# Performance work log

Measured on AMD Instinct MI355X. Metric: run time of the kernel, lower is better.

## Reference

```python
import jax, jax.numpy as jnp
import numpy as np

B, M, H, R = 4096, 4, 1024, 10
MID, D3 = 512, 3 * H  # gate MLP mid = max(32, H//2)
AUDIO = 1
OTHERS = (0, 2, 3)


def _ln(x, w, b):
    m = jnp.mean(x, axis=-1, keepdims=True)
    v = jnp.mean((x - m) ** 2, axis=-1, keepdims=True)
    return (x - m) * jax.lax.rsqrt(v + 1e-5) * w + b


def _gate(t, s, lw, lb, w1, b1, w2, b2):
    feat = jnp.concatenate([t, s, jnp.abs(t - s)], axis=-1)  # [..., 3H]
    h = jax.nn.gelu(_ln(feat, lw, lb) @ w1.T + b1, approximate=False)
    return jax.nn.sigmoid(h @ w2.T + b2)  # [..., 1]


def setup_inputs() -> dict:
    key = jax.random.key(0)
    ks = jax.random.split(key, 16)
    xn = lambda k, shp, fan: jax.random.normal(k, shp, jnp.float32) * (1.0 / np.sqrt(fan))
    inp = {
        'tokens': jax.random.normal(ks[0], (B, M, H), jnp.float32),
        'token_mask': jax.random.randint(ks[1], (B, M), 0, 2) > 0,
        # gate_other: LayerNorm(3H) -> Linear(3H,MID) -> GELU -> Linear(MID,1)
        'ln_go_w': jnp.ones((D3,), jnp.float32), 'ln_go_b': jnp.zeros((D3,), jnp.float32),
        'go_w1': xn(ks[2], (MID, D3), D3), 'go_b1': jnp.zeros((MID,), jnp.float32),
        'go_w2': xn(ks[3], (1, MID), MID), 'go_b2': jnp.zeros((1,), jnp.float32),
        # gate_audio
        'ln_ga_w': jnp.ones((D3,), jnp.float32), 'ln_ga_b': jnp.zeros((D3,), jnp.float32),
        'ga_w1': xn(ks[4], (MID, D3), D3), 'ga_b1': jnp.zeros((MID,), jnp.float32),
        'ga_w2': xn(ks[5], (1, MID), MID), 'ga_b2': jnp.zeros((1,), jnp.float32),
        'a2o_w': xn(ks[6], (H, H), H), 'o2a_w': xn(ks[7], (H, H), H),
        'ln_o_w': jnp.ones((H,), jnp.float32), 'ln_o_b': jnp.zeros((H,), jnp.float32),
        'ln_a_w': jnp.ones((H,), jnp.float32), 'ln_a_b': jnp.zeros((H,), jnp.float32),
        # LMF
        'factors': jax.random.normal(ks[8], (M, R, H + 1, H), jnp.float32) * np.sqrt(2.0 / (H + 1 + H)),
        'rank_w': jax.random.normal(ks[9], (R,), jnp.float32) * 0.02,
        'lmf_bias': jnp.zeros((H,), jnp.float32),
        'out_ln1_w': jnp.ones((H,), jnp.float32), 'out_ln1_b': jnp.zeros((H,), jnp.float32),
        'out_w': xn(ks[10], (H, H), H), 'out_b': jnp.zeros((H,), jnp.float32),
        'out_ln2_w': jnp.ones((H,), jnp.float32), 'out_ln2_b': jnp.zeros((H,), jnp.float32),
    }
    return inp


def reference(tokens, token_mask, ln_go_w, ln_go_b, go_w1, go_b1, go_w2, go_b2,
              ln_ga_w, ln_ga_b, ga_w1, ga_b1, ga_w2, ga_b2, a2o_w, o2a_w,
              ln_o_w, ln_o_b, ln_a_w, ln_a_b, factors, rank_w, lmf_bias,
              out_ln1_w, out_ln1_b, out_w, out_b, out_ln2_w, out_ln2_b):
    mask_f = token_mask.astype(tokens.dtype)  # [B, M]
    oidx = jnp.asarray(OTHERS)

    # ---- AudioGuidedResidualMixer (eval mode) ----
    audio = tokens[:, AUDIO]                          # [B, H]
    audio_valid = token_mask[:, AUDIO]                # [B]
    others = tokens[:, oidx] * mask_f[:, oidx, None]  # [B, 3, H] (masked targets)
    src = jnp.broadcast_to(audio[:, None, :], others.shape)
    g = _gate(others, src, ln_go_w, ln_go_b, go_w1, go_b1, go_w2, go_b2)  # [B,3,1]
    a2o = audio @ a2o_w.T                                                  # [B, H]
    upd = _ln(others + g * a2o[:, None, :], ln_o_w, ln_o_b)
    pair_valid = token_mask[:, oidx] & audio_valid[:, None]                # [B, 3]
    others_new = jnp.where(pair_valid[..., None], upd, others) * mask_f[:, oidx, None]

    w_o = mask_f[:, oidx, None]
    denom = jnp.clip(w_o.sum(axis=1), 1.0, None)
    others_mean = (others_new * w_o).sum(axis=1) / denom                   # [B, H]
    aum = audio_valid & token_mask[:, oidx].any(axis=1)                    # [B]
    g_a = _gate(audio, others_mean, ln_ga_w, ln_ga_b, ga_w1, ga_b1, ga_w2, ga_b2)
    o2a = others_mean @ o2a_w.T
    mixed_audio = jnp.where(aum[:, None],
                            _ln(audio + g_a * o2a, ln_a_w, ln_a_b),
                            audio * mask_f[:, AUDIO, None])
    mixed = jnp.stack([others_new[:, 0], mixed_audio, others_new[:, 1], others_new[:, 2]],
                      axis=1) * mask_f[..., None]                          # [B, M, H]

    # ---- LowRankMultiplicativeFusion ----
    one = jnp.ones((mixed.shape[0], M, 1), mixed.dtype)
    x_aug = jnp.concatenate([one, mixed], axis=-1)                         # [B, M, H+1]
    z = jnp.einsum('bmd,mrdh->bmrh', x_aug, factors)                       # [B, M, R, H]
    z = jnp.where(token_mask[:, :, None, None], z, jnp.ones((), z.dtype))
    rank_tensor = jnp.prod(z, axis=1)                                      # [B, R, H]
    fused = jnp.einsum('brh,r->bh', rank_tensor, rank_w) + lmf_bias
    h = _ln(fused, out_ln1_w, out_ln1_b)
    h = jax.nn.gelu(h @ out_w.T + out_b, approximate=False)
    return _ln(h, out_ln2_w, out_ln2_b)                                    # [B, H]
```

## Files before the change

### kernel.cpp

```cpp
#include <hip/hip_runtime.h>
#include <math.h>

#define BB 4096
#define HH 1024
#define RR 10
#define MIDD 512
#define D3 3072

typedef __bf16 bf16x8 __attribute__((ext_vector_type(8)));
typedef __bf16 bf16x4 __attribute__((ext_vector_type(4)));
typedef float f32x4 __attribute__((ext_vector_type(4)));

__device__ __forceinline__ float waveSum(float v){
#pragma unroll
  for(int o=32;o>0;o>>=1) v += __shfl_down(v,o,64);
  return v;
}
__device__ __forceinline__ float blockSum256(float v, float* sc){
  v = waveSum(v);
  __syncthreads();
  if((threadIdx.x & 63)==0) sc[threadIdx.x>>6] = v;
  __syncthreads();
  return sc[0]+sc[1]+sc[2]+sc[3];
}
__device__ __forceinline__ float gelu_f(float x){
  return 0.5f*x*(1.0f+erff(x*0.70710678118654752f));
}
__device__ __forceinline__ void gl_lds16(const void* g, void* lds){
  __builtin_amdgcn_global_load_lds((const __attribute__((address_space(1))) unsigned int*)g,
                                   (__attribute__((address_space(3))) unsigned int*)lds,
                                   16, 0, 0);
}

__global__ void convw_k(const float* __restrict__ s0, __bf16* __restrict__ d0, int n0,
                        const float* __restrict__ s1, __bf16* __restrict__ d1, int n1,
                        const float* __restrict__ s2, __bf16* __restrict__ d2, int n2,
                        const float* __restrict__ s3, __bf16* __restrict__ d3, int n3,
                        const float* __restrict__ s4, __bf16* __restrict__ d4, int n4){
  long i = ((long)blockIdx.x*256 + threadIdx.x)*4;
  const float* s; __bf16* d;
  if(i<n0){ s=s0; d=d0; }
  else { i-=n0; if(i<n1){ s=s1; d=d1; }
  else { i-=n1; if(i<n2){ s=s2; d=d2; }
  else { i-=n2; if(i<n3){ s=s3; d=d3; }
  else { i-=n3; if(i>=n4) return; s=s4; d=d4; } } } }
  float4 v=*(const float4*)(s+i);
  bf16x4 o; o[0]=(__bf16)v.x; o[1]=(__bf16)v.y; o[2]=(__bf16)v.z; o[3]=(__bf16)v.w;
  *(bf16x4*)(d+i)=o;
}

__global__ void feat_go_k(const float* __restrict__ tokens, const int* __restrict__ mask,
                          const float* __restrict__ lnw, const float* __restrict__ lnb,
                          __bf16* __restrict__ featGo, __bf16* __restrict__ audioB){
  int row=blockIdx.x; int b=row/3; int j=row-b*3; int oj=(j==0)?0:(j+1);
  const float* to=tokens+((size_t)b*4+oj)*HH;
  const float* ta=tokens+((size_t)b*4+1)*HH;
  float mo = mask[b*4+oj]?1.f:0.f;
  int tid=threadIdx.x;
  __shared__ float sc[4];
  float ov[4], av[4], dv[4]; float s=0.f,s2=0.f;
#pragma unroll
  for(int p=0;p<4;p++){
    int h=tid+p*256;
    float o=to[h]*mo, a=ta[h], d=fabsf(o-a);
    ov[p]=o; av[p]=a; dv[p]=d;
    s+=o+a+d; s2+=o*o+a*a+d*d;
  }
  s=blockSum256(s,sc); s2=blockSum256(s2,sc);
  float mean=s/(float)D3, rstd=rsqrtf(s2/(float)D3-mean*mean+1e-5f);
  __bf16* fr = featGo + (size_t)row*D3;
#pragma unroll
  for(int p=0;p<4;p++){
    int h=tid+p*256;
    fr[h]       =(__bf16)((ov[p]-mean)*rstd*lnw[h]+lnb[h]);
    fr[1024+h]  =(__bf16)((av[p]-mean)*rstd*lnw[1024+h]+lnb[1024+h]);
    fr[2048+h]  =(__bf16)((dv[p]-mean)*rstd*lnw[2048+h]+lnb[2048+h]);
    if(j==0) audioB[(size_t)b*HH+h]=(__bf16)av[p];
  }
}

__global__ void feat_ga_k(const float* __restrict__ tokens, const float* __restrict__ omean,
                          const float* __restrict__ lnw, const float* __restrict__ lnb,
                          __bf16* __restrict__ featGa){
  int b=blockIdx.x; int tid=threadIdx.x;
  const float* ta=tokens+((size_t)b*4+1)*HH;
  const float* so=omean+(size_t)b*HH;
  __shared__ float sc[4];
  float tv[4], sv[4], dv[4]; float s=0.f,s2=0.f;
#pragma unroll
  for(int p=0;p<4;p++){
    int h=tid+p*256;
    float a=ta[h], o=so[h], d=fabsf(a-o);
    tv[p]=a; sv[p]=o; dv[p]=d;
    s+=a+o+d; s2+=a*a+o*o+d*d;
  }
  s=blockSum256(s,sc); s2=blockSum256(s2,sc);
  float mean=s/(float)D3, rstd=rsqrtf(s2/(float)D3-mean*mean+1e-5f);
  __bf16* fr = featGa + (size_t)b*D3;
#pragma unroll
  for(int p=0;p<4;p++){
    int h=tid+p*256;
    fr[h]     =(__bf16)((tv[p]-mean)*rstd*lnw[h]+lnb[h]);
    fr[1024+h]=(__bf16)((sv[p]-mean)*rstd*lnw[1024+h]+lnb[1024+h]);
    fr[2048+h]=(__bf16)((dv[p]-mean)*rstd*lnw[2048+h]+lnb[2048+h]);
  }
}

template<int ACT>
__launch_bounds__(256, 2)
__global__ void gemm_nt_mfma(const __bf16* __restrict__ A, int lda,
                             const __bf16* __restrict__ Bm, int ldb,
                             const float* __restrict__ bias,
                             float* __restrict__ C, int ldc, int K){
  __shared__ __align__(16) __bf16 As[128*32];
  __shared__ __align__(16) __bf16 Bs[128*32];
  const int tid=threadIdx.x, l=tid&63, w=tid>>6;
  const int wr=w>>1, wc=w&1;
  const int quad=l>>4, lr16=l&15;
  const int row0=blockIdx.y*128, col0=blockIdx.x*128;
  const int srow=l>>2, sq=(l&3)^((l>>3)&3);
  f32x4 acc[4][4];
  f32x4 zerov={0.f,0.f,0.f,0.f};
#pragma unroll
  for(int i=0;i<4;i++)
#pragma unroll
    for(int j=0;j<4;j++) acc[i][j]=zerov;
  for(int k0=0;k0<K;k0+=32){
    __syncthreads();
#pragma unroll
    for(int t=0;t<2;t++){
      int ch=w+4*t;
      gl_lds16(A  + (size_t)(row0+ch*16+srow)*lda + k0 + sq*8, As + (size_t)(ch*64+l)*8);
      gl_lds16(Bm + (size_t)(col0+ch*16+srow)*ldb + k0 + sq*8, Bs + (size_t)(ch*64+l)*8);
    }
    __syncthreads();
    bf16x8 af[4], bg[4];
#pragma unroll
    for(int fi=0;fi<4;fi++){
      int R=wr*64+fi*16+lr16;
      af[fi]=*(const bf16x8*)(As + R*32 + ((quad^(R>>1))&3)*8);
    }
#pragma unroll
    for(int fj=0;fj<4;fj++){
      int N=wc*64+fj*16+lr16;
      bg[fj]=*(const bf16x8*)(Bs + N*32 + ((quad^(N>>1))&3)*8);
    }
#pragma unroll
    for(int fi=0;fi<4;fi++)
#pragma unroll
      for(int fj=0;fj<4;fj++)
        acc[fi][fj]=__builtin_amdgcn_mfma_f32_16x16x32_bf16(af[fi],bg[fj],acc[fi][fj],0,0,0);
  }
  float bv[4];
#pragma unroll
  for(int fj=0;fj<4;fj++) bv[fj] = (ACT==1)? bias[col0+wc*64+fj*16+lr16] : 0.f;
#pragma unroll
  for(int fi=0;fi<4;fi++){
#pragma unroll
    for(int reg=0;reg<4;reg++){
      int row=row0+wr*64+fi*16+quad*4+reg;
#pragma unroll
      for(int fj=0;fj<4;fj++){
        int col=col0+wc*64+fj*16+lr16;
        float v=acc[fi][fj][reg];
        if(ACT==1) v=gelu_f(v+bv[fj]);
        C[(size_t)row*ldc+col]=v;
      }
    }
  }
}

__global__ void gate_reduce_k(const float* __restrict__ Hx, const float* __restrict__ w2,
                              const float* __restrict__ b2, float* __restrict__ g, int cols){
  int row=blockIdx.x;
  float s=0.f;
  for(int c=threadIdx.x;c<cols;c+=64) s += Hx[(size_t)row*cols+c]*w2[c];
  s=waveSum(s);
  if(threadIdx.x==0) g[row]=1.f/(1.f+expf(-(s+b2[0])));
}

__global__ void others_k(const float* __restrict__ tokens, const int* __restrict__ mask,
                         const float* __restrict__ g, const float* __restrict__ a2o,
                         const float* __restrict__ lnw, const float* __restrict__ lnb,
                         __bf16* __restrict__ mixedB, float* __restrict__ omean,
                         __bf16* __restrict__ omeanB){
  int b=blockIdx.x, tid=threadIdx.x;
  __shared__ float sc[4];
  float ma = mask[b*4+1]?1.f:0.f;
  float a2[4];
#pragma unroll
  for(int p=0;p<4;p++) a2[p]=a2o[(size_t)b*HH+tid+p*256];
  float sum[4]={0,0,0,0}; float cnt=0.f;
  for(int j=0;j<3;j++){
    int oj=(j==0)?0:(j+1);
    float mo=mask[b*4+oj]?1.f:0.f; cnt+=mo;
    float gv=g[b*3+j];
    float t[4], ov[4]; float s=0.f,s2=0.f;
#pragma unroll
    for(int p=0;p<4;p++){
      int h=tid+p*256;
      float o=tokens[((size_t)b*4+oj)*HH+h]*mo;
      ov[p]=o; t[p]=o+gv*a2[p];
      s+=t[p]; s2+=t[p]*t[p];
    }
    s=blockSum256(s,sc); s2=blockSum256(s2,sc);
    float mean=s/1024.f, rstd=rsqrtf(s2/1024.f-mean*mean+1e-5f);
    float pv=mo*ma;
#pragma unroll
    for(int p=0;p<4;p++){
      int h=tid+p*256;
      float upd=(t[p]-mean)*rstd*lnw[h]+lnb[h];
      float on=((pv>0.5f)?upd:ov[p])*mo;
      mixedB[(size_t)b*4096 + (size_t)oj*HH + h]=(__bf16)on;
      sum[p]+=on*mo;
    }
  }
  float denom=fmaxf(cnt,1.f);
#pragma unroll
  for(int p=0;p<4;p++){
    float v=sum[p]/denom;
    omean[(size_t)b*HH+tid+p*256]=v;
    omeanB[(size_t)b*HH+tid+p*256]=(__bf16)v;
  }
}

__global__ void audio_k(const float* __restrict__ tokens, const int* __restrict__ mask,
                        const float* __restrict__ g_a, const float* __restrict__ o2a,
                        const float* __restrict__ lnw, const float* __restrict__ lnb,
                        __bf16* __restrict__ mixedB){
  int b=blockIdx.x, tid=threadIdx.x;
  __shared__ float sc[4];
  int ma_i=mask[b*4+1];
  int any = mask[b*4+0]|mask[b*4+2]|mask[b*4+3];
  bool aum = (ma_i!=0) && (any!=0);
  float ma = ma_i?1.f:0.f;
  float gv=g_a[b];
  const float* ta = tokens + ((size_t)b*4+1)*HH;
  float av[4], t[4]; float s=0.f,s2=0.f;
#pragma unroll
  for(int p=0;p<4;p++){
    int h=tid+p*256;
    av[p]=ta[h];
    t[p]=av[p]+gv*o2a[(size_t)b*HH+h];
    s+=t[p]; s2+=t[p]*t[p];
  }
  s=blockSum256(s,sc); s2=blockSum256(s2,sc);
  float mean=s/1024.f, rstd=rsqrtf(s2/1024.f-mean*mean+1e-5f);
#pragma unroll
  for(int p=0;p<4;p++){
    int h=tid+p*256;
    float u=(t[p]-mean)*rstd*lnw[h]+lnb[h];
    float outv = aum ? u : av[p]*ma;
    mixedB[(size_t)b*4096 + HH + h]=(__bf16)(outv*ma);
  }
}

__global__ void transpose_factors_k(const float* __restrict__ factors,
                                    __bf16* __restrict__ factT){
  __shared__ float T[64][65];
  int mr = blockIdx.z;
  int d0 = blockIdx.y*64, h0 = blockIdx.x*64;
  int t = threadIdx.x;
  int rr = t>>4, cc = (t&15)*4;
  const float* src = factors + ((size_t)mr*1025 + 1 + d0)*1024 + h0;
#pragma unroll
  for(int q=0;q<4;q++){
    float4 v = *(const float4*)(src + (size_t)(q*16+rr)*1024 + cc);
    T[q*16+rr][cc]=v.x; T[q*16+rr][cc+1]=v.y; T[q*16+rr][cc+2]=v.z; T[q*16+rr][cc+3]=v.w;
  }
  __syncthreads();
  __bf16* dst = factT + ((size_t)mr*1024 + h0)*1024 + d0;
#pragma unroll
  for(int q=0;q<4;q++){
    int hr = q*16 + rr;
    bf16x4 o;
    o[0]=(__bf16)T[cc][hr];   o[1]=(__bf16)T[cc+1][hr];
    o[2]=(__bf16)T[cc+2][hr]; o[3]=(__bf16)T[cc+3][hr];
    *(bf16x4*)(dst + (size_t)hr*1024 + cc) = o;
  }
}

__launch_bounds__(256, 2)
__global__ void gemm_lmf_mfma(const __bf16* __restrict__ mixedB,
                              const __bf16* __restrict__ factT,
                              const float* __restrict__ factors,
                              const int* __restrict__ mask,
                              float* __restrict__ P){
  __shared__ __align__(16) __bf16 As[3*4096];
  __shared__ __align__(16) __bf16 Bs[3*4096];
  __shared__ float Mskf[4][128];
  __shared__ float F0s[4][128];
  const int tid = threadIdx.x;
  const int l = tid & 63, w = tid >> 6;
  const int wr = w >> 1, wc = w & 1;
  const int quad = l >> 4, lr16 = l & 15;

  const int flat = blockIdx.x + 8*(blockIdx.y + 32*blockIdx.z);
  const int nid  = (flat & 7)*320 + (flat >> 3);
  const int bx   = nid & 7;
  const int rest = nid >> 3;
  const int by   = rest & 31;
  const int r    = rest >> 5;
  const int row0 = by * 128, col0 = bx * 128;

  const int srow = l >> 2;
  const int sq   = (l & 3) ^ ((l >> 3) & 3);

  for(int i = tid; i < 512; i += 256){
    int mm = i >> 7, rl = i & 127;
    Mskf[mm][rl] = mask[(row0 + rl)*4 + mm] ? 1.f : 0.f;
    F0s[mm][rl]  = factors[(size_t)(mm*RR + r)*1025*1024 + col0 + rl];
  }

  const __bf16* pa0 = mixedB + (size_t)(row0 + w*16     + srow)*4096 + sq*8;
  const __bf16* pa1 = mixedB + (size_t)(row0 + (w+4)*16 + srow)*4096 + sq*8;
  const __bf16* pb0 = factT + ((size_t)r*1024 + col0 + w*16     + srow)*1024 + sq*8;
  const __bf16* pb1 = factT + ((size_t)r*1024 + col0 + (w+4)*16 + srow)*1024 + sq*8;
  __bf16* da0 = As + ((size_t)w*64     + l)*8;
  __bf16* da1 = As + ((size_t)(w+4)*64 + l)*8;
  __bf16* db0 = Bs + ((size_t)w*64     + l)*8;
  __bf16* db1 = Bs + ((size_t)(w+4)*64 + l)*8;

  auto stage = [&](int s, int bi){
    int mm = s >> 5; int k0 = (s & 31)*32;
    size_t ao = (size_t)mm*1024 + k0;
    size_t bo = (size_t)mm*(RR*1048576) + k0;
    gl_lds16(pa0 + ao, da0 + bi*4096);
    gl_lds16(pa1 + ao, da1 + bi*4096);
    gl_lds16(pb0 + bo, db0 + bi*4096);
    gl_lds16(pb1 + bo, db1 + bi*4096);
  };

  f32x4 prod[4][4];
  f32x4 onev = {1.f,1.f,1.f,1.f};
#pragma unroll
  for(int i=0;i<4;i++)
#pragma unroll
    for(int j=0;j<4;j++) prod[i][j] = onev;

  stage(0, 0);
  stage(1, 1);
  asm volatile("s_waitcnt vmcnt(4)" ::: "memory");
  asm volatile("s_waitcnt lgkmcnt(0)" ::: "memory");
  __builtin_amdgcn_s_barrier();

  f32x4 acc[4][4];
  int cur = 0;
  for(int step = 0; step < 128; ++step){
    const __bf16* Ab = As + cur*4096;
    const __bf16* Bb = Bs + cur*4096;
    bf16x8 af[4], bg[4];
#pragma unroll
    for(int fi=0;fi<4;fi++){
      int R = wr*64 + fi*16 + lr16;
      af[fi] = *(const bf16x8*)(Ab + R*32 + ((quad ^ (R>>1)) & 3)*8);
    }
#pragma unroll
    for(int fj=0;fj<4;fj++){
      int N = wc*64 + fj*16 + lr16;
      bg[fj] = *(const bf16x8*)(Bb + N*32 + ((quad ^ (N>>1)) & 3)*8);
    }
    if(step + 2 < 128){
      int bi = cur + 2; if(bi >= 3) bi -= 3;
      stage(step + 2, bi);
    }
    if((step & 31) == 0){
      int mm = step >> 5;
#pragma unroll
      for(int fj=0;fj<4;fj++){
        float f0 = F0s[mm][wc*64 + fj*16 + lr16];
        f32x4 iv = {f0,f0,f0,f0};
#pragma unroll
        for(int fi=0;fi<4;fi++) acc[fi][fj] = iv;
      }
    }
    __builtin_amdgcn_s_setprio(1);
#pragma unroll
    for(int fi=0;fi<4;fi++)
#pragma unroll
      for(int fj=0;fj<4;fj++)
        acc[fi][fj] = __builtin_amdgcn_mfma_f32_16x16x32_bf16(af[fi], bg[fj], acc[fi][fj], 0,0,0);
    __builtin_amdgcn_s_setprio(0);
    if((step & 31) == 31){
      int mm = step >> 5;
#pragma unroll
      for(int fi=0;fi<4;fi++)
#pragma unroll
        for(int reg=0;reg<4;reg++){
          float mk = Mskf[mm][wr*64 + fi*16 + quad*4 + reg];
#pragma unroll
          for(int fj=0;fj<4;fj++)
            prod[fi][fj][reg] *= (mk != 0.f) ? acc[fi][fj][reg] : 1.f;
        }
    }
    asm volatile("s_waitcnt lgkmcnt(0)" ::: "memory");
    if(step < 126) asm volatile("s_waitcnt vmcnt(4)" ::: "memory");
    else           asm volatile("s_waitcnt vmcnt(0)" ::: "memory");
    __builtin_amdgcn_s_barrier();
    cur = (cur + 1 == 3) ? 0 : cur + 1;
  }

#pragma unroll
  for(int fi=0;fi<4;fi++){
#pragma unroll
    for(int reg=0;reg<4;reg++){
      int row = row0 + wr*64 + fi*16 + quad*4 + reg;
#pragma unroll
      for(int fj=0;fj<4;fj++){
        int col = col0 + wc*64 + fj*16 + lr16;
        P[((size_t)row*RR + r)*HH + col] = prod[fi][fj][reg];
      }
    }
  }
}

__global__ void fuse_k(const float* __restrict__ P, const float* __restrict__ rank_w,
                       const float* __restrict__ lmf_bias, float* __restrict__ fused){
  size_t i=(size_t)blockIdx.x*256+threadIdx.x;
  int b=(int)(i>>10), h=(int)(i&1023);
  float s=lmf_bias[h];
#pragma unroll
  for(int r=0;r<RR;r++) s += rank_w[r]*P[((size_t)b*RR+r)*HH+h];
  fused[i]=s;
}

__global__ void ln_row_k(const float* __restrict__ X, const float* __restrict__ w,
                         const float* __restrict__ bb, float* __restrict__ Y){
  int b=blockIdx.x, tid=threadIdx.x;
  __shared__ float sc[4];
  const float* x=X+(size_t)b*HH;
  float t[4]; float s=0.f,s2=0.f;
#pragma unroll
  for(int p=0;p<4;p++){ t[p]=x[tid+p*256]; s+=t[p]; s2+=t[p]*t[p]; }
  s=blockSum256(s,sc); s2=blockSum256(s2,sc);
  float mean=s/1024.f, rstd=rsqrtf(s2/1024.f-mean*mean+1e-5f);
#pragma unroll
  for(int p=0;p<4;p++){
    int h=tid+p*256;
    Y[(size_t)b*HH+h]=(t[p]-mean)*rstd*w[h]+bb[h];
  }
}
__global__ void ln_row_bf16_k(const float* __restrict__ X, const float* __restrict__ w,
                              const float* __restrict__ bb, __bf16* __restrict__ Y){
  int b=blockIdx.x, tid=threadIdx.x;
  __shared__ float sc[4];
  const float* x=X+(size_t)b*HH;
  float t[4]; float s=0.f,s2=0.f;
#pragma unroll
  for(int p=0;p<4;p++){ t[p]=x[tid+p*256]; s+=t[p]; s2+=t[p]*t[p]; }
  s=blockSum256(s,sc); s2=blockSum256(s2,sc);
  float mean=s/1024.f, rstd=rsqrtf(s2/1024.f-mean*mean+1e-5f);
#pragma unroll
  for(int p=0;p<4;p++){
    int h=tid+p*256;
    Y[(size_t)b*HH+h]=(__bf16)((t[p]-mean)*rstd*w[h]+bb[h]);
  }
}

extern "C" void kernel_launch(void* const* d_in, const int* in_sizes, int n_in,
                              void* d_out, int out_size, void* d_ws, size_t ws_size,
                              hipStream_t stream) {
  const float* tokens   =(const float*)d_in[0];
  const int*   mask     =(const int*)  d_in[1];
  const float* ln_go_w  =(const float*)d_in[2];
  const float* ln_go_b  =(const float*)d_in[3];
  const float* go_w1    =(const float*)d_in[4];
  const float* go_b1    =(const float*)d_in[5];
  const float* go_w2    =(const float*)d_in[6];
  const float* go_b2    =(const float*)d_in[7];
  const float* ln_ga_w  =(const float*)d_in[8];
  const float* ln_ga_b  =(const float*)d_in[9];
  const float* ga_w1    =(const float*)d_in[10];
  const float* ga_b1    =(const float*)d_in[11];
  const float* ga_w2    =(const float*)d_in[12];
  const float* ga_b2    =(const float*)d_in[13];
  const float* a2o_w    =(const float*)d_in[14];
  const float* o2a_w    =(const float*)d_in[15];
  const float* ln_o_w   =(const float*)d_in[16];
  const float* ln_o_b   =(const float*)d_in[17];
  const float* ln_a_w   =(const float*)d_in[18];
  const float* ln_a_b   =(const float*)d_in[19];
  const float* factors  =(const float*)d_in[20];
  const float* rank_w   =(const float*)d_in[21];
  const float* lmf_bias =(const float*)d_in[22];
  const float* out_ln1_w=(const float*)d_in[23];
  const float* out_ln1_b=(const float*)d_in[24];
  const float* out_w    =(const float*)d_in[25];
  const float* out_b    =(const float*)d_in[26];
  const float* out_ln2_w=(const float*)d_in[27];
  const float* out_ln2_b=(const float*)d_in[28];
  float* out=(float*)d_out;

  char* wsp=(char*)d_ws; size_t off=0;
  auto alloc=[&](size_t bytes)->void*{
    void* p=wsp+off; off=(off+bytes+255)&~(size_t)255; return p;
  };
  float*  P       =(float*) alloc((size_t)BB*RR*HH*4);
  __bf16* factT   =(__bf16*)alloc((size_t)4*RR*HH*HH*2);
  float*  H1      =(float*) alloc((size_t)BB*3*MIDD*4);
  float*  g_go    =(float*) alloc((size_t)BB*3*4);
  float*  a2o     =(float*) alloc((size_t)BB*HH*4);
  __bf16* mixedB  =(__bf16*)alloc((size_t)BB*4*HH*2);
  float*  omean   =(float*) alloc((size_t)BB*HH*4);
  __bf16* omeanB  =(__bf16*)alloc((size_t)BB*HH*2);
  __bf16* audioB  =(__bf16*)alloc((size_t)BB*HH*2);
  float*  H2      =(float*) alloc((size_t)BB*MIDD*4);
  float*  g_a     =(float*) alloc((size_t)BB*4);
  float*  o2a     =(float*) alloc((size_t)BB*HH*4);
  float*  fused   =(float*) alloc((size_t)BB*HH*4);
  __bf16* hbufB   =(__bf16*)alloc((size_t)BB*HH*2);
  __bf16* go_w1B  =(__bf16*)alloc((size_t)MIDD*D3*2);
  __bf16* ga_w1B  =(__bf16*)alloc((size_t)MIDD*D3*2);
  __bf16* a2o_wB  =(__bf16*)alloc((size_t)HH*HH*2);
  __bf16* o2a_wB  =(__bf16*)alloc((size_t)HH*HH*2);
  __bf16* out_wB  =(__bf16*)alloc((size_t)HH*HH*2);
  __bf16* featGo  =(__bf16*)P;
  __bf16* featGa  =(__bf16*)((char*)P + (size_t)BB*3*D3*2);

  {
    int n0=MIDD*D3, n1=MIDD*D3, n2=HH*HH, n3=HH*HH, n4=HH*HH;
    int total4=(n0+n1+n2+n3+n4)/4;
    convw_k<<<(total4+255)/256,256,0,stream>>>(go_w1,go_w1B,n0, ga_w1,ga_w1B,n1,
                                               a2o_w,a2o_wB,n2, o2a_w,o2a_wB,n3,
                                               out_w,out_wB,n4);
  }
  transpose_factors_k<<<dim3(16,16,40),256,0,stream>>>(factors,factT);
  feat_go_k<<<BB*3,256,0,stream>>>(tokens,mask,ln_go_w,ln_go_b,featGo,audioB);
  gemm_nt_mfma<0><<<dim3(8,32),256,0,stream>>>(audioB,HH,a2o_wB,HH,nullptr,a2o,HH,HH);
  gemm_nt_mfma<1><<<dim3(4,96),256,0,stream>>>(featGo,D3,go_w1B,D3,go_b1,H1,MIDD,D3);
  gate_reduce_k<<<BB*3,64,0,stream>>>(H1,go_w2,go_b2,g_go,MIDD);
  others_k<<<BB,256,0,stream>>>(tokens,mask,g_go,a2o,ln_o_w,ln_o_b,mixedB,omean,omeanB);
  feat_ga_k<<<BB,256,0,stream>>>(tokens,omean,ln_ga_w,ln_ga_b,featGa);
  gemm_nt_mfma<1><<<dim3(4,32),256,0,stream>>>(featGa,D3,ga_w1B,D3,ga_b1,H2,MIDD,D3);
  gate_reduce_k<<<BB,64,0,stream>>>(H2,ga_w2,ga_b2,g_a,MIDD);
  gemm_nt_mfma<0><<<dim3(8,32),256,0,stream>>>(omeanB,HH,o2a_wB,HH,nullptr,o2a,HH,HH);
  audio_k<<<BB,256,0,stream>>>(tokens,mask,g_a,o2a,ln_a_w,ln_a_b,mixedB);
  gemm_lmf_mfma<<<dim3(HH/128,BB/128,RR),256,0,stream>>>(mixedB,factT,factors,mask,P);
  fuse_k<<<(BB*HH)/256,256,0,stream>>>(P,rank_w,lmf_bias,fused);
  ln_row_bf16_k<<<BB,256,0,stream>>>(fused,out_ln1_w,out_ln1_b,hbufB);
  gemm_nt_mfma<1><<<dim3(8,32),256,0,stream>>>(hbufB,HH,out_wB,HH,out_b,fused,HH,HH);
  ln_row_k<<<BB,256,0,stream>>>(fused,out_ln2_w,out_ln2_b,out);
}
```

Measured before the change: 1.126 ms.

## Pipeline generic GEMM with triple-buffered LDS, 64-row tiles, and fuse rank-sum into LN

```diff
diff --git a/kernel.cpp b/kernel.cpp
--- a/kernel.cpp
+++ b/kernel.cpp
@@ -107,58 +107,94 @@
 }
 
 template<int ACT>
-__launch_bounds__(256, 2)
+__launch_bounds__(256, 4)
 __global__ void gemm_nt_mfma(const __bf16* __restrict__ A, int lda,
                              const __bf16* __restrict__ Bm, int ldb,
                              const float* __restrict__ bias,
                              float* __restrict__ C, int ldc, int K){
-  __shared__ __align__(16) __bf16 As[128*32];
-  __shared__ __align__(16) __bf16 Bs[128*32];
+  __shared__ __align__(16) __bf16 As[3*2048];
+  __shared__ __align__(16) __bf16 Bs[3*4096];
   const int tid=threadIdx.x, l=tid&63, w=tid>>6;
   const int wr=w>>1, wc=w&1;
   const int quad=l>>4, lr16=l&15;
-  const int row0=blockIdx.y*128, col0=blockIdx.x*128;
+
+  const int nbx = gridDim.x;
+  const int flat = blockIdx.x + nbx*blockIdx.y;
+  const int chunk = (nbx*gridDim.y)>>3;
+  const int nid = (flat&7)*chunk + (flat>>3);
+  const int bx = nid % nbx, by = nid / nbx;
+  const int row0=by*64, col0=bx*128;
+
   const int srow=l>>2, sq=(l&3)^((l>>3)&3);
-  f32x4 acc[4][4];
+  const int nsteps = K>>5;
+
+  const __bf16* pa  = A  + (size_t)(row0 + w*16       + srow)*lda + sq*8;
+  const __bf16* pb0 = Bm + (size_t)(col0 + w*16       + srow)*ldb + sq*8;
+  const __bf16* pb1 = Bm + (size_t)(col0 + (w+4)*16   + srow)*ldb + sq*8;
+  __bf16* da  = As + ((size_t)w*64     + l)*8;
+  __bf16* db0 = Bs + ((size_t)w*64     + l)*8;
+  __bf16* db1 = Bs + ((size_t)(w+4)*64 + l)*8;
+
+  auto stage=[&](int s,int bi){
+    int k0 = s*32;
+    gl_lds16(pa  + k0, da  + bi*2048);
+    gl_lds16(pb0 + k0, db0 + bi*4096);
+    gl_lds16(pb1 + k0, db1 + bi*4096);
+  };
+
+  f32x4 acc[2][4];
   f32x4 zerov={0.f,0.f,0.f,0.f};
 #pragma unroll
-  for(int i=0;i<4;i++)
+  for(int i=0;i<2;i++)
 #pragma unroll
     for(int j=0;j<4;j++) acc[i][j]=zerov;
-  for(int k0=0;k0<K;k0+=32){
-    __syncthreads();
-#pragma unroll
-    for(int t=0;t<2;t++){
-      int ch=w+4*t;
-      gl_lds16(A  + (size_t)(row0+ch*16+srow)*lda + k0 + sq*8, As + (size_t)(ch*64+l)*8);
-      gl_lds16(Bm + (size_t)(col0+ch*16+srow)*ldb + k0 + sq*8, Bs + (size_t)(ch*64+l)*8);
-    }
-    __syncthreads();
-    bf16x8 af[4], bg[4];
-#pragma unroll
-    for(int fi=0;fi<4;fi++){
-      int R=wr*64+fi*16+lr16;
-      af[fi]=*(const bf16x8*)(As + R*32 + ((quad^(R>>1))&3)*8);
+
+  stage(0,0);
+  stage(1,1);
+  asm volatile("s_waitcnt vmcnt(3)" ::: "memory");
+  __builtin_amdgcn_s_barrier();
+
+  int cur=0;
+  for(int step=0; step<nsteps; ++step){
+    const __bf16* Ab = As + cur*2048;
+    const __bf16* Bb = Bs + cur*4096;
+    bf16x8 af[2], bg[4];
+#pragma unroll
+    for(int fi=0;fi<2;fi++){
+      int R = wr*32 + fi*16 + lr16;
+      af[fi]=*(const bf16x8*)(Ab + R*32 + ((quad^(R>>1))&3)*8);
     }
 #pragma unroll
     for(int fj=0;fj<4;fj++){
-      int N=wc*64+fj*16+lr16;
-      bg[fj]=*(const bf16x8*)(Bs + N*32 + ((quad^(N>>1))&3)*8);
-    }
-#pragma unroll
-    for(int fi=0;fi<4;fi++)
+      int N = wc*64 + fj*16 + lr16;
+      bg[fj]=*(const bf16x8*)(Bb + N*32 + ((quad^(N>>1))&3)*8);
+    }
+    if(step+2<nsteps){
+      int bi = cur + 2; if(bi>=3) bi-=3;
+      stage(step+2, bi);
+    }
+    __builtin_amdgcn_s_setprio(1);
+#pragma unroll
+    for(int fi=0;fi<2;fi++)
 #pragma unroll
       for(int fj=0;fj<4;fj++)
         acc[fi][fj]=__builtin_amdgcn_mfma_f32_16x16x32_bf16(af[fi],bg[fj],acc[fi][fj],0,0,0);
-  }
+    __builtin_amdgcn_s_setprio(0);
+    asm volatile("s_waitcnt lgkmcnt(0)" ::: "memory");
+    if(step < nsteps-2) asm volatile("s_waitcnt vmcnt(3)" ::: "memory");
+    else                asm volatile("s_waitcnt vmcnt(0)" ::: "memory");
+    __builtin_amdgcn_s_barrier();
+    cur = (cur+1==3)?0:cur+1;
+  }
+
   float bv[4];
 #pragma unroll
   for(int fj=0;fj<4;fj++) bv[fj] = (ACT==1)? bias[col0+wc*64+fj*16+lr16] : 0.f;
 #pragma unroll
-  for(int fi=0;fi<4;fi++){
+  for(int fi=0;fi<2;fi++){
 #pragma unroll
     for(int reg=0;reg<4;reg++){
-      int row=row0+wr*64+fi*16+quad*4+reg;
+      int row=row0+wr*32+fi*16+quad*4+reg;
 #pragma unroll
       for(int fj=0;fj<4;fj++){
         int col=col0+wc*64+fj*16+lr16;
@@ -414,14 +450,32 @@
   }
 }
 
-__global__ void fuse_k(const float* __restrict__ P, const float* __restrict__ rank_w,
-                       const float* __restrict__ lmf_bias, float* __restrict__ fused){
-  size_t i=(size_t)blockIdx.x*256+threadIdx.x;
-  int b=(int)(i>>10), h=(int)(i&1023);
-  float s=lmf_bias[h];
-#pragma unroll
-  for(int r=0;r<RR;r++) s += rank_w[r]*P[((size_t)b*RR+r)*HH+h];
-  fused[i]=s;
+__global__ void fuse_ln_k(const float* __restrict__ P, const float* __restrict__ rank_w,
+                          const float* __restrict__ lmf_bias,
+                          const float* __restrict__ w, const float* __restrict__ bb,
+                          __bf16* __restrict__ Y){
+  int b=blockIdx.x, tid=threadIdx.x;
+  __shared__ float sc[4];
+  float rw[RR];
+#pragma unroll
+  for(int r=0;r<RR;r++) rw[r]=rank_w[r];
+  const float* Pb = P + (size_t)b*RR*HH;
+  float t[4]; float s=0.f,s2=0.f;
+#pragma unroll
+  for(int p=0;p<4;p++){
+    int h=tid+p*256;
+    float v=lmf_bias[h];
+#pragma unroll
+    for(int r=0;r<RR;r++) v += rw[r]*Pb[(size_t)r*HH+h];
+    t[p]=v; s+=v; s2+=v*v;
+  }
+  s=blockSum256(s,sc); s2=blockSum256(s2,sc);
+  float mean=s/1024.f, rstd=rsqrtf(s2/1024.f-mean*mean+1e-5f);
+#pragma unroll
+  for(int p=0;p<4;p++){
+    int h=tid+p*256;
+    Y[(size_t)b*HH+h]=(__bf16)((t[p]-mean)*rstd*w[h]+bb[h]);
+  }
 }
 
 __global__ void ln_row_k(const float* __restrict__ X, const float* __restrict__ w,
@@ -438,22 +492,6 @@
   for(int p=0;p<4;p++){
     int h=tid+p*256;
     Y[(size_t)b*HH+h]=(t[p]-mean)*rstd*w[h]+bb[h];
-  }
-}
-__global__ void ln_row_bf16_k(const float* __restrict__ X, const float* __restrict__ w,
-                              const float* __restrict__ bb, __bf16* __restrict__ Y){
-  int b=blockIdx.x, tid=threadIdx.x;
-  __shared__ float sc[4];
-  const float* x=X+(size_t)b*HH;
-  float t[4]; float s=0.f,s2=0.f;
-#pragma unroll
-  for(int p=0;p<4;p++){ t[p]=x[tid+p*256]; s+=t[p]; s2+=t[p]*t[p]; }
-  s=blockSum256(s,sc); s2=blockSum256(s2,sc);
-  float mean=s/1024.f, rstd=rsqrtf(s2/1024.f-mean*mean+1e-5f);
-#pragma unroll
-  for(int p=0;p<4;p++){
-    int h=tid+p*256;
-    Y[(size_t)b*HH+h]=(__bf16)((t[p]-mean)*rstd*w[h]+bb[h]);
   }
 }
 
@@ -526,18 +564,17 @@
   }
   transpose_factors_k<<<dim3(16,16,40),256,0,stream>>>(factors,factT);
   feat_go_k<<<BB*3,256,0,stream>>>(tokens,mask,ln_go_w,ln_go_b,featGo,audioB);
-  gemm_nt_mfma<0><<<dim3(8,32),256,0,stream>>>(audioB,HH,a2o_wB,HH,nullptr,a2o,HH,HH);
-  gemm_nt_mfma<1><<<dim3(4,96),256,0,stream>>>(featGo,D3,go_w1B,D3,go_b1,H1,MIDD,D3);
+  gemm_nt_mfma<0><<<dim3(8,64),256,0,stream>>>(audioB,HH,a2o_wB,HH,nullptr,a2o,HH,HH);
+  gemm_nt_mfma<1><<<dim3(4,192),256,0,stream>>>(featGo,D3,go_w1B,D3,go_b1,H1,MIDD,D3);
   gate_reduce_k<<<BB*3,64,0,stream>>>(H1,go_w2,go_b2,g_go,MIDD);
   others_k<<<BB,256,0,stream>>>(tokens,mask,g_go,a2o,ln_o_w,ln_o_b,mixedB,omean,omeanB);
   feat_ga_k<<<BB,256,0,stream>>>(tokens,omean,ln_ga_w,ln_ga_b,featGa);
-  gemm_nt_mfma<1><<<dim3(4,32),256,0,stream>>>(featGa,D3,ga_w1B,D3,ga_b1,H2,MIDD,D3);
+  gemm_nt_mfma<1><<<dim3(4,64),256,0,stream>>>(featGa,D3,ga_w1B,D3,ga_b1,H2,MIDD,D3);
   gate_reduce_k<<<BB,64,0,stream>>>(H2,ga_w2,ga_b2,g_a,MIDD);
-  gemm_nt_mfma<0><<<dim3(8,32),256,0,stream>>>(omeanB,HH,o2a_wB,HH,nullptr,o2a,HH,HH);
+  gemm_nt_mfma<0><<<dim3(8,64),256,0,stream>>>(omeanB,HH,o2a_wB,HH,nullptr,o2a,HH,HH);
   audio_k<<<BB,256,0,stream>>>(tokens,mask,g_a,o2a,ln_a_w,ln_a_b,mixedB);
   gemm_lmf_mfma<<<dim3(HH/128,BB/128,RR),256,0,stream>>>(mixedB,factT,factors,mask,P);
-  fuse_k<<<(BB*HH)/256,256,0,stream>>>(P,rank_w,lmf_bias,fused);
-  ln_row_bf16_k<<<BB,256,0,stream>>>(fused,out_ln1_w,out_ln1_b,hbufB);
-  gemm_nt_mfma<1><<<dim3(8,32),256,0,stream>>>(hbufB,HH,out_wB,HH,out_b,fused,HH,HH);
+  fuse_ln_k<<<BB,256,0,stream>>>(P,rank_w,lmf_bias,out_ln1_w,out_ln1_b,hbufB);
+  gemm_nt_mfma<1><<<dim3(8,64),256,0,stream>>>(hbufB,HH,out_wB,HH,out_b,fused,HH,HH);
   ln_row_k<<<BB,256,0,stream>>>(fused,out_ln2_w,out_ln2_b,out);
 }
```

Result: faster. 1.031 ms (-8.4%).
